# Kernel optimization log

Measured on AMD Instinct MI355X. Metric: run time of the kernel, lower is better.

Reference implementation:

```python
import jax, jax.numpy as jnp
import numpy as np

N, E, F_IN, H, C = 50000, 800000, 128, 4, 32
NEG_SLOPE = 0.2
BN_EPS = 1e-5


def setup_inputs() -> dict:
    key = jax.random.key(0)
    ks = jax.random.split(key, 6)
    x = jax.random.normal(ks[0], (N, F_IN), dtype=jnp.float32)
    edge_index = jax.random.randint(ks[1], (2, E), 0, N, dtype=jnp.int64)
    W = jax.random.normal(ks[2], (H * C, F_IN), dtype=jnp.float32) * (1.0 / np.sqrt(F_IN))
    att_src = jax.random.normal(ks[3], (H, C), dtype=jnp.float32) * 0.1
    att_dst = jax.random.normal(ks[4], (H, C), dtype=jnp.float32) * 0.1
    bias = jnp.zeros((H * C,), dtype=jnp.float32)
    gamma = jnp.ones((H * C,), dtype=jnp.float32)
    beta = jnp.zeros((H * C,), dtype=jnp.float32)
    return {"x": x, "edge_index": edge_index, "W": W, "att_src": att_src,
            "att_dst": att_dst, "bias": bias, "gamma": gamma, "beta": beta}


def reference(x, edge_index, W, att_src, att_dst, bias, gamma, beta):
    n = x.shape[0]
    loop = jnp.arange(n, dtype=edge_index.dtype)
    src = jnp.concatenate([edge_index[0], loop])  # add_self_loops=True (PyG default)
    dst = jnp.concatenate([edge_index[1], loop])
    # Linear projection (lin has no bias in GATConv)
    h = (x @ W.T).reshape(n, H, C)                      # [N,H,C]
    a_src = jnp.einsum('nhc,hc->nh', h, att_src)        # [N,H]
    a_dst = jnp.einsum('nhc,hc->nh', h, att_dst)
    e = jax.nn.leaky_relu(a_src[src] + a_dst[dst], NEG_SLOPE)  # [E+N,H]
    # segment softmax over incoming edges of each dst node
    emax = jax.ops.segment_max(e, dst, num_segments=n)
    emax = jnp.where(jnp.isfinite(emax), emax, 0.0)
    ex = jnp.exp(e - emax[dst])
    denom = jax.ops.segment_sum(ex, dst, num_segments=n)
    alpha = ex / (denom[dst] + 1e-16)                   # [E+N,H]
    msg = h[src] * alpha[:, :, None]                    # [E+N,H,C]
    out = jax.ops.segment_sum(msg, dst, num_segments=n).reshape(n, H * C) + bias
    out = jax.nn.relu(out)
    # BatchNorm1d over node dimension (training-mode batch stats)
    mean = out.mean(axis=0)
    var = out.var(axis=0)
    out = (out - mean) * jax.lax.rsqrt(var + BN_EPS) * gamma + beta
    return out
```

## Files before the change

kernel.cpp:

```cpp
#include <hip/hip_runtime.h>
#include <hip/hip_bf16.h>

#define HEADS 4
#define FDIM 128
#define NEG_SLOPE 0.2f
#define BN_EPS 1e-5f
#define CAP 3072
#define NB 512
#define NSLOT 32

typedef __attribute__((ext_vector_type(8))) short s8v;
typedef __attribute__((ext_vector_type(4))) float f4v;

__device__ __forceinline__ float lrelu(float x) { return x >= 0.f ? x : NEG_SLOPE * x; }

__device__ __forceinline__ unsigned short f2bf(float f) {
    unsigned int u = __float_as_uint(f);
    unsigned int r = (u + 0x7fffu + ((u >> 16) & 1u)) >> 16;
    return (unsigned short)r;
}
__device__ __forceinline__ float bflo(unsigned int u) { return __uint_as_float(u << 16); }
__device__ __forceinline__ float bfhi(unsigned int u) { return __uint_as_float(u & 0xffff0000u); }

__global__ __launch_bounds__(256) void k1_gemm_count(
    const float* __restrict__ x, const float* __restrict__ W,
    const float* __restrict__ att_src, const float* __restrict__ att_dst,
    const int* __restrict__ ei,
    unsigned short* __restrict__ hb, float* __restrict__ a_src,
    float* __restrict__ a_dst, int* __restrict__ cnts,
    int n, int E, int nbuk, int cpb, int gb)
{
    __shared__ uint4 bsh[2048];
    __shared__ int shi[512];
    int t = threadIdx.x;

    if ((int)blockIdx.x >= gb) {
        int cbid = blockIdx.x - gb;
        for (int i = t; i < nbuk; i += 256) shi[i] = 0;
        __syncthreads();
        int e0 = cbid * cpb, e1 = min(E, e0 + cpb);
        for (int e = e0 + t; e < e1; e += 256) atomicAdd(&shi[ei[E + e] >> 7], 1);
        __syncthreads();
        for (int i = t; i < nbuk; i += 256) cnts[cbid * nbuk + i] = shi[i];
        return;
    }

    for (int i = t; i < 2048; i += 256) {
        int l = i & 63, kt = (i >> 6) & 3, nt = i >> 8;
        int nrow = nt * 16 + (l & 15);
        int kb = kt * 32 + ((l >> 4) << 3);
        const float* src = W + nrow * FDIM + kb;
        float4 f0 = *(const float4*)src, f1 = *(const float4*)(src + 4);
        unsigned u0 = f2bf(f0.x) | ((unsigned)f2bf(f0.y) << 16);
        unsigned u1 = f2bf(f0.z) | ((unsigned)f2bf(f0.w) << 16);
        unsigned u2 = f2bf(f1.x) | ((unsigned)f2bf(f1.y) << 16);
        unsigned u3 = f2bf(f1.z) | ((unsigned)f2bf(f1.w) << 16);
        bsh[i] = make_uint4(u0, u1, u2, u3);
    }
    __syncthreads();

    int l = t & 63, wid = t >> 6;
    int r_base = blockIdx.x * 64 + wid * 16;
    int rg = l >> 4, l15 = l & 15;
    int row_in = r_base + l15;
    int rd = row_in < n ? row_in : 0;

    f4v acc[8];
#pragma unroll
    for (int i = 0; i < 8; ++i) acc[i] = (f4v){0.f, 0.f, 0.f, 0.f};
#pragma unroll
    for (int kt = 0; kt < 4; ++kt) {
        const float4* xp = (const float4*)(x + (size_t)rd * FDIM + kt * 32 + (rg << 3));
        float4 f0 = xp[0], f1 = xp[1];
        s8v a;
        a[0] = (short)f2bf(f0.x); a[1] = (short)f2bf(f0.y);
        a[2] = (short)f2bf(f0.z); a[3] = (short)f2bf(f0.w);
        a[4] = (short)f2bf(f1.x); a[5] = (short)f2bf(f1.y);
        a[6] = (short)f2bf(f1.z); a[7] = (short)f2bf(f1.w);
#pragma unroll
        for (int nt = 0; nt < 8; ++nt) {
            s8v b = *(const s8v*)&bsh[(nt * 4 + kt) * 64 + l];
            acc[nt] = __builtin_amdgcn_mfma_f32_16x16x32_bf16(a, b, acc[nt], 0, 0, 0);
        }
    }

    float asv[8], adv[8];
#pragma unroll
    for (int nt = 0; nt < 8; ++nt) {
        asv[nt] = att_src[nt * 16 + l15];
        adv[nt] = att_dst[nt * 16 + l15];
    }
#pragma unroll
    for (int r = 0; r < 4; ++r) {
        int row = r_base + rg * 4 + r;
        float ps[HEADS], pd[HEADS];
#pragma unroll
        for (int h = 0; h < HEADS; ++h) {
            ps[h] = acc[2 * h][r] * asv[2 * h] + acc[2 * h + 1][r] * asv[2 * h + 1];
            pd[h] = acc[2 * h][r] * adv[2 * h] + acc[2 * h + 1][r] * adv[2 * h + 1];
        }
#pragma unroll
        for (int d = 1; d < 16; d <<= 1) {
#pragma unroll
            for (int h = 0; h < HEADS; ++h) {
                ps[h] += __shfl_xor(ps[h], d);
                pd[h] += __shfl_xor(pd[h], d);
            }
        }
        if (l15 == 0 && row < n) {
            *(float4*)&a_src[row * HEADS] = make_float4(ps[0], ps[1], ps[2], ps[3]);
            *(float4*)&a_dst[row * HEADS] = make_float4(pd[0], pd[1], pd[2], pd[3]);
        }
    }
#pragma unroll
    for (int nt = 0; nt < 8; ++nt) {
#pragma unroll
        for (int r = 0; r < 4; ++r) {
            int row = r_base + rg * 4 + r;
            if (row < n) hb[(size_t)row * FDIM + nt * 16 + l15] = f2bf(acc[nt][r]);
        }
    }
}

__global__ __launch_bounds__(256) void k2_scanblk(const int* __restrict__ cnts,
                                                  int* __restrict__ bases,
                                                  int* __restrict__ sizes, int nbuk) {
    __shared__ int tmp[512];
    int b = blockIdx.x, t = threadIdx.x;
    int v0 = cnts[t * nbuk + b];
    int v1 = cnts[(t + 256) * nbuk + b];
    tmp[t] = v0; tmp[t + 256] = v1;
    __syncthreads();
    for (int s = 1; s < 512; s <<= 1) {
        int x0 = (t >= s) ? tmp[t - s] : 0;
        int x1 = (t + 256 >= s) ? tmp[t + 256 - s] : 0;
        __syncthreads();
        tmp[t] += x0; tmp[t + 256] += x1;
        __syncthreads();
    }
    bases[t * nbuk + b] = tmp[t] - v0;
    bases[(t + 256) * nbuk + b] = tmp[t + 256] - v1;
    if (t == 255) sizes[b] = tmp[511];
}

__global__ __launch_bounds__(1024) void k3_bucket_scan(
    const int* __restrict__ ei, const int* __restrict__ bases,
    const int* __restrict__ sizes, unsigned int* __restrict__ bucketed,
    int* __restrict__ goffs, int* __restrict__ offs,
    float* __restrict__ slotbuf,
    int N, int E, int nbuk, int cpb)
{
    __shared__ int lb[512];
    __shared__ int lr[512];
    int t = threadIdx.x;
    if ((int)blockIdx.x == NB) {
        int v = 0;
        if (t < 512) { v = (t < nbuk) ? sizes[t] : 0; lb[t] = v; }
        __syncthreads();
        for (int s = 1; s < 512; s <<= 1) {
            int x = (t < 512 && t >= s) ? lb[t - s] : 0;
            __syncthreads();
            if (t < 512) lb[t] += x;
            __syncthreads();
        }
        if (t < nbuk) goffs[t] = lb[t] - v;
        if (t == 0) { goffs[nbuk] = E; offs[N] = E; }
        for (int i = t; i < NSLOT * 256; i += 1024) slotbuf[i] = 0.f;
        return;
    }
    int bid = blockIdx.x;
    for (int i = t; i < nbuk; i += 1024) { lb[i] = bases[bid * nbuk + i]; lr[i] = 0; }
    __syncthreads();
    int e0 = bid * cpb, e1 = min(E, e0 + cpb);
    for (int e = e0 + t; e < e1; e += 1024) {
        int s = ei[e], d = ei[E + e];
        int b = d >> 7;
        int r = atomicAdd(&lr[b], 1);
        int p = lb[b] + r;
        if (p < CAP)
            bucketed[(size_t)b * CAP + p] = ((unsigned)(d & 127) << 16) | (unsigned)s;
    }
}

__global__ __launch_bounds__(256) void k4_csr(const unsigned int* __restrict__ bucketed,
                                              const int* __restrict__ sizes,
                                              const int* __restrict__ goffs,
                                              int* __restrict__ offs,
                                              unsigned short* __restrict__ csr, int N) {
    __shared__ int cnt[512], loff[512], tmp[512];
    int b = blockIdx.x, t = threadIdx.x;
    int sz = min(sizes[b], CAP), gbase = goffs[b];
    cnt[t] = 0; cnt[t + 256] = 0;
    __syncthreads();
    const unsigned int* seg = bucketed + (size_t)b * CAP;
    for (int j = t; j < sz; j += 256) {
        unsigned rec = seg[j];
        int key = (int)((rec >> 16) << 2) | (int)((rec & 0xffffu) >> 14);
        atomicAdd(&cnt[key], 1);
    }
    __syncthreads();
    tmp[t] = cnt[t]; tmp[t + 256] = cnt[t + 256];
    __syncthreads();
    for (int s = 1; s < 512; s <<= 1) {
        int x0 = (t >= s) ? tmp[t - s] : 0;
        int x1 = (t + 256 >= s) ? tmp[t + 256 - s] : 0;
        __syncthreads();
        tmp[t] += x0; tmp[t + 256] += x1;
        __syncthreads();
    }
    loff[t] = tmp[t] - cnt[t];
    loff[t + 256] = tmp[t + 256] - cnt[t + 256];
    if (t < 128) {
        int node = b * 128 + t;
        if (node < N) offs[node] = gbase + tmp[4 * t] - cnt[4 * t];
    }
    __syncthreads();
    for (int j = t; j < sz; j += 256) {
        unsigned rec = seg[j];
        int src = (int)(rec & 0xffffu);
        int key = (int)((rec >> 16) << 2) | (src >> 14);
        int pos = atomicAdd(&loff[key], 1);
        csr[gbase + pos] = (unsigned short)src;
    }
}

#define AGG_E(S, EW)                                                         \
    {                                                                        \
        uint4 u_ = *(const uint4*)&hb[(size_t)(S) * FDIM + c8];              \
        acc0.x += (EW) * bflo(u_.x); acc0.y += (EW) * bfhi(u_.x);            \
        acc0.z += (EW) * bflo(u_.y); acc0.w += (EW) * bfhi(u_.y);            \
        acc1.x += (EW) * bflo(u_.z); acc1.y += (EW) * bfhi(u_.z);            \
        acc1.z += (EW) * bflo(u_.w); acc1.w += (EW) * bfhi(u_.w);            \
        denom += (EW);                                                       \
    }

#define ACC2(E0, U0, E1, U1)                                                 \
    acc0.x += (E0) * bflo((U0).x) + (E1) * bflo((U1).x);                     \
    acc0.y += (E0) * bfhi((U0).x) + (E1) * bfhi((U1).x);                     \
    acc0.z += (E0) * bflo((U0).y) + (E1) * bflo((U1).y);                     \
    acc0.w += (E0) * bfhi((U0).y) + (E1) * bfhi((U1).y);                     \
    acc1.x += (E0) * bflo((U0).z) + (E1) * bflo((U1).z);                     \
    acc1.y += (E0) * bfhi((U0).z) + (E1) * bfhi((U1).z);                     \
    acc1.z += (E0) * bflo((U0).w) + (E1) * bflo((U1).w);                     \
    acc1.w += (E0) * bfhi((U0).w) + (E1) * bfhi((U1).w);

__global__ __launch_bounds__(256) void k5_agg(
    const unsigned short* __restrict__ hb, const float* __restrict__ a_src,
    const float* __restrict__ a_dst, const int* __restrict__ offs,
    const unsigned short* __restrict__ csr, const float* __restrict__ bias,
    unsigned short* __restrict__ outb, int n)
{
    int lane = threadIdx.x & 63;
    int node = blockIdx.x * 4 + (threadIdx.x >> 6);
    if (node >= n) return;
    int g = lane >> 4;
    int q = lane & 15;
    int c8 = q * 8;
    int head = q >> 2;

    float ad = a_dst[node * HEADS + head];
    int beg = offs[node], end = offs[node + 1];

    float4 acc0 = make_float4(0.f, 0.f, 0.f, 0.f);
    float4 acc1 = make_float4(0.f, 0.f, 0.f, 0.f);
    float denom = 0.f;

    if (g == 0) {
        float e_ = __expf(lrelu(a_src[node * HEADS + head] + ad));
        AGG_E(node, e_);
    }

    int j = beg + g;
    for (; j + 12 < end; j += 16) {
        int s0 = csr[j], s1 = csr[j + 4], s2 = csr[j + 8], s3 = csr[j + 12];
        float A0 = a_src[s0 * HEADS + head];
        float A1 = a_src[s1 * HEADS + head];
        float A2 = a_src[s2 * HEADS + head];
        float A3 = a_src[s3 * HEADS + head];
        uint4 u0 = *(const uint4*)&hb[(size_t)s0 * FDIM + c8];
        uint4 u1 = *(const uint4*)&hb[(size_t)s1 * FDIM + c8];
        uint4 u2 = *(const uint4*)&hb[(size_t)s2 * FDIM + c8];
        uint4 u3 = *(const uint4*)&hb[(size_t)s3 * FDIM + c8];
        float e0 = __expf(lrelu(A0 + ad));
        float e1 = __expf(lrelu(A1 + ad));
        float e2 = __expf(lrelu(A2 + ad));
        float e3 = __expf(lrelu(A3 + ad));
        ACC2(e0, u0, e1, u1);
        ACC2(e2, u2, e3, u3);
        denom += e0 + e1 + e2 + e3;
    }
    for (; j + 4 < end; j += 8) {
        int s0 = csr[j], s1 = csr[j + 4];
        float A0 = a_src[s0 * HEADS + head];
        float A1 = a_src[s1 * HEADS + head];
        uint4 u0 = *(const uint4*)&hb[(size_t)s0 * FDIM + c8];
        uint4 u1 = *(const uint4*)&hb[(size_t)s1 * FDIM + c8];
        float e0 = __expf(lrelu(A0 + ad));
        float e1 = __expf(lrelu(A1 + ad));
        ACC2(e0, u0, e1, u1);
        denom += e0 + e1;
    }
    for (; j < end; j += 4) {
        int s0 = csr[j];
        float e0 = __expf(lrelu(a_src[s0 * HEADS + head] + ad));
        AGG_E(s0, e0);
    }

#pragma unroll
    for (int d = 16; d < 64; d <<= 1) {
        acc0.x += __shfl_xor(acc0.x, d);
        acc0.y += __shfl_xor(acc0.y, d);
        acc0.z += __shfl_xor(acc0.z, d);
        acc0.w += __shfl_xor(acc0.w, d);
        acc1.x += __shfl_xor(acc1.x, d);
        acc1.y += __shfl_xor(acc1.y, d);
        acc1.z += __shfl_xor(acc1.z, d);
        acc1.w += __shfl_xor(acc1.w, d);
        denom += __shfl_xor(denom, d);
    }

    if (g == 0) {
        float inv = 1.f / (denom + 1e-16f);
        float4 b0 = *(const float4*)&bias[c8];
        float4 b1 = *(const float4*)&bias[c8 + 4];
        float o0 = fmaxf(acc0.x * inv + b0.x, 0.f);
        float o1 = fmaxf(acc0.y * inv + b0.y, 0.f);
        float o2 = fmaxf(acc0.z * inv + b0.z, 0.f);
        float o3 = fmaxf(acc0.w * inv + b0.w, 0.f);
        float o4 = fmaxf(acc1.x * inv + b1.x, 0.f);
        float o5 = fmaxf(acc1.y * inv + b1.y, 0.f);
        float o6 = fmaxf(acc1.z * inv + b1.z, 0.f);
        float o7 = fmaxf(acc1.w * inv + b1.w, 0.f);
        uint4 p;
        p.x = (unsigned)f2bf(o0) | ((unsigned)f2bf(o1) << 16);
        p.y = (unsigned)f2bf(o2) | ((unsigned)f2bf(o3) << 16);
        p.z = (unsigned)f2bf(o4) | ((unsigned)f2bf(o5) << 16);
        p.w = (unsigned)f2bf(o6) | ((unsigned)f2bf(o7) << 16);
        ((uint4*)outb)[(size_t)node * 16 + q] = p;
    }
}

__global__ __launch_bounds__(256) void bn_sums(const unsigned short* __restrict__ outb,
                                               float* __restrict__ slotbuf, int n) {
    int t = threadIdx.x;
    int q = t & 31, rh = t >> 5;
    float4 s = make_float4(0.f, 0.f, 0.f, 0.f);
    float4 s2 = make_float4(0.f, 0.f, 0.f, 0.f);
    const uint2* o2 = (const uint2*)outb;
    for (int r = blockIdx.x * 8 + rh; r < n; r += gridDim.x * 8) {
        uint2 u = o2[(size_t)r * 32 + q];
        float4 v = make_float4(bflo(u.x), bfhi(u.x), bflo(u.y), bfhi(u.y));
        s.x += v.x; s.y += v.y; s.z += v.z; s.w += v.w;
        s2.x += v.x * v.x; s2.y += v.y * v.y; s2.z += v.z * v.z; s2.w += v.w * v.w;
    }
    __shared__ float4 sh[2][8][32];
    sh[0][rh][q] = s;
    sh[1][rh][q] = s2;
    __syncthreads();
    if (rh == 0) {
#pragma unroll
        for (int i = 1; i < 8; ++i) {
            float4 a = sh[0][i][q], b = sh[1][i][q];
            s.x += a.x; s.y += a.y; s.z += a.z; s.w += a.w;
            s2.x += b.x; s2.y += b.y; s2.z += b.z; s2.w += b.w;
        }
        float* slot = slotbuf + (blockIdx.x & (NSLOT - 1)) * 256;
        atomicAdd(&slot[q * 4 + 0], s.x);
        atomicAdd(&slot[q * 4 + 1], s.y);
        atomicAdd(&slot[q * 4 + 2], s.z);
        atomicAdd(&slot[q * 4 + 3], s.w);
        atomicAdd(&slot[128 + q * 4 + 0], s2.x);
        atomicAdd(&slot[128 + q * 4 + 1], s2.y);
        atomicAdd(&slot[128 + q * 4 + 2], s2.z);
        atomicAdd(&slot[128 + q * 4 + 3], s2.w);
    }
}

__global__ __launch_bounds__(256) void k6_bn_apply(
    float* __restrict__ out, const unsigned short* __restrict__ outb,
    const float* __restrict__ slotbuf,
    const float* __restrict__ gamma, const float* __restrict__ beta, int N)
{
    __shared__ __align__(16) float sc[FDIM], sh[FDIM];
    int t = threadIdx.x;
    if (t < FDIM) {
        float s = 0.f, s2 = 0.f;
#pragma unroll
        for (int k = 0; k < NSLOT; ++k) {
            s  += slotbuf[k * 256 + t];
            s2 += slotbuf[k * 256 + 128 + t];
        }
        float mean = s / (float)N;
        float var = fmaxf(s2 / (float)N - mean * mean, 0.f);
        float g = gamma[t] * rsqrtf(var + BN_EPS);
        sc[t] = g;
        sh[t] = beta[t] - mean * g;
    }
    __syncthreads();
    int n4 = N * 32;
    const uint2* o2 = (const uint2*)outb;
    for (int i = blockIdx.x * 256 + t; i < n4; i += gridDim.x * 256) {
        uint2 u = o2[i];
        float4 v = make_float4(bflo(u.x), bfhi(u.x), bflo(u.y), bfhi(u.y));
        int f = (i & 31) * 4;
        float4 s4 = *(const float4*)&sc[f];
        float4 h4 = *(const float4*)&sh[f];
        v.x = v.x * s4.x + h4.x;
        v.y = v.y * s4.y + h4.y;
        v.z = v.z * s4.z + h4.z;
        v.w = v.w * s4.w + h4.w;
        ((float4*)out)[i] = v;
    }
}

static inline size_t align256(size_t x) { return (x + 255) & ~(size_t)255; }

extern "C" void kernel_launch(void* const* d_in, const int* in_sizes, int n_in,
                              void* d_out, int out_size, void* d_ws, size_t ws_size,
                              hipStream_t stream) {
    const float* x       = (const float*)d_in[0];
    const int*   ei      = (const int*)d_in[1];
    const float* W       = (const float*)d_in[2];
    const float* att_src = (const float*)d_in[3];
    const float* att_dst = (const float*)d_in[4];
    const float* bias    = (const float*)d_in[5];
    const float* gamma   = (const float*)d_in[6];
    const float* beta    = (const float*)d_in[7];
    float* out = (float*)d_out;

    int N = in_sizes[0] / FDIM;
    int E = in_sizes[1] / 2;
    int nbuk = (N + 127) >> 7;
    int cpb = (E + NB - 1) / NB;
    int gb = (N + 63) / 64;

    char* w = (char*)d_ws;
    unsigned short* hb = (unsigned short*)w;  w += align256((size_t)N * FDIM * 2);
    float* a_src  = (float*)w;  w += align256((size_t)N * HEADS * 4);
    float* a_dst  = (float*)w;  w += align256((size_t)N * HEADS * 4);
    int*   offs   = (int*)w;    w += align256((size_t)(N + 1) * 4);
    int*   cnts   = (int*)w;    w += align256((size_t)NB * nbuk * 4);
    int*   bases  = (int*)w;    w += align256((size_t)NB * nbuk * 4);
    int*   sizes  = (int*)w;    w += align256((size_t)nbuk * 4);
    int*   goffs  = (int*)w;    w += align256((size_t)(nbuk + 1) * 4);
    unsigned int* bucketed = (unsigned int*)w;  w += align256((size_t)nbuk * CAP * 4);
    unsigned short* csr = (unsigned short*)w;   w += align256((size_t)E * 2);
    unsigned short* outb = (unsigned short*)w;  w += align256((size_t)N * FDIM * 2);
    float* slotbuf = (float*)w; w += align256((size_t)NSLOT * 256 * 4);

    k1_gemm_count<<<gb + NB, 256, 0, stream>>>(x, W, att_src, att_dst, ei,
                                               hb, a_src, a_dst, cnts,
                                               N, E, nbuk, cpb, gb);
    k2_scanblk<<<nbuk, 256, 0, stream>>>(cnts, bases, sizes, nbuk);
    k3_bucket_scan<<<NB + 1, 1024, 0, stream>>>(ei, bases, sizes, bucketed,
                                                goffs, offs, slotbuf,
                                                N, E, nbuk, cpb);
    k4_csr<<<nbuk, 256, 0, stream>>>(bucketed, sizes, goffs, offs, csr, N);
    k5_agg<<<(N + 3) / 4, 256, 0, stream>>>(hb, a_src, a_dst, offs, csr, bias, outb, N);
    bn_sums<<<512, 256, 0, stream>>>(outb, slotbuf, N);
    k6_bn_apply<<<2048, 256, 0, stream>>>(out, outb, slotbuf, gamma, beta, N);
}
```

Measured before the change: 97.96 us.

## Fuse BN statistics into aggregation, locally sort bucket scatter, simplify CSR build

The BatchNorm sum and sum-of-squares accumulation moves into the aggregation kernel through a shared-memory reduction plus slot atomics. This removes the separate bn_sums pass that re-read the output, and a tiny finalize kernel now computes scale and shift. The bucket scatter first sorts each block's edges by bucket in shared memory so global writes land contiguously. The CSR kernel now keys on destination node only (128 bins) rather than node plus source high bits, which shrinks its scan but drops the within-node ordering by source. NSLOT doubles to cut atomic contention, at the cost of 12500 blocks hitting atomics and a CSR order that may lose locality.

After: 116.5 us. +19.0%, slower.

```diff
diff --git a/kernel.cpp b/kernel.cpp
--- a/kernel.cpp
+++ b/kernel.cpp
@@ -7,7 +7,7 @@
 #define BN_EPS 1e-5f
 #define CAP 3072
 #define NB 512
-#define NSLOT 32
+#define NSLOT 64
 
 typedef __attribute__((ext_vector_type(8))) short s8v;
 typedef __attribute__((ext_vector_type(4))) float f4v;
@@ -151,7 +151,10 @@
     int N, int E, int nbuk, int cpb)
 {
     __shared__ int lb[512];
-    __shared__ int lr[512];
+    __shared__ int cnt[512];
+    __shared__ int bscan[512];
+    __shared__ int loff[512];
+    __shared__ unsigned recs[2048];
     int t = threadIdx.x;
     if ((int)blockIdx.x == NB) {
         int v = 0;
@@ -169,16 +172,45 @@
         return;
     }
     int bid = blockIdx.x;
-    for (int i = t; i < nbuk; i += 1024) { lb[i] = bases[bid * nbuk + i]; lr[i] = 0; }
+    if (t < 512) {
+        lb[t] = (t < nbuk) ? bases[bid * nbuk + t] : 0;
+        cnt[t] = 0;
+    }
     __syncthreads();
     int e0 = bid * cpb, e1 = min(E, e0 + cpb);
+    int szblk = e1 - e0;
+    unsigned myrec[2]; int myb[2]; int nmine = 0;
     for (int e = e0 + t; e < e1; e += 1024) {
         int s = ei[e], d = ei[E + e];
         int b = d >> 7;
-        int r = atomicAdd(&lr[b], 1);
-        int p = lb[b] + r;
+        myrec[nmine] = ((unsigned)b << 23) | ((unsigned)(d & 127) << 16) | (unsigned)s;
+        myb[nmine] = b;
+        ++nmine;
+        atomicAdd(&cnt[b], 1);
+    }
+    __syncthreads();
+    if (t < 512) bscan[t] = cnt[t];
+    __syncthreads();
+    for (int s = 1; s < 512; s <<= 1) {
+        int x = (t < 512 && t >= s) ? bscan[t - s] : 0;
+        __syncthreads();
+        if (t < 512) bscan[t] += x;
+        __syncthreads();
+    }
+    if (t < 512) loff[t] = bscan[t] - cnt[t];
+    __syncthreads();
+    for (int k = 0; k < nmine; ++k) {
+        int pos = atomicAdd(&loff[myb[k]], 1);
+        recs[pos] = myrec[k];
+    }
+    __syncthreads();
+    for (int i = t; i < szblk; i += 1024) {
+        unsigned rec = recs[i];
+        int b = rec >> 23;
+        int local = i - (bscan[b] - cnt[b]);
+        int p = lb[b] + local;
         if (p < CAP)
-            bucketed[(size_t)b * CAP + p] = ((unsigned)(d & 127) << 16) | (unsigned)s;
+            bucketed[(size_t)b * CAP + p] = rec & 0x7fffffu;
     }
 }
 
@@ -187,40 +219,33 @@
                                               const int* __restrict__ goffs,
                                               int* __restrict__ offs,
                                               unsigned short* __restrict__ csr, int N) {
-    __shared__ int cnt[512], loff[512], tmp[512];
+    __shared__ int cnt[128], loff[128], tmp[128];
     int b = blockIdx.x, t = threadIdx.x;
     int sz = min(sizes[b], CAP), gbase = goffs[b];
-    cnt[t] = 0; cnt[t + 256] = 0;
+    if (t < 128) cnt[t] = 0;
     __syncthreads();
     const unsigned int* seg = bucketed + (size_t)b * CAP;
+    for (int j = t; j < sz; j += 256) atomicAdd(&cnt[(seg[j] >> 16) & 127], 1);
+    __syncthreads();
+    if (t < 128) tmp[t] = cnt[t];
+    __syncthreads();
+    for (int s = 1; s < 128; s <<= 1) {
+        int x = (t < 128 && t >= s) ? tmp[t - s] : 0;
+        __syncthreads();
+        if (t < 128) tmp[t] += x;
+        __syncthreads();
+    }
+    if (t < 128) {
+        loff[t] = tmp[t] - cnt[t];
+        int node = b * 128 + t;
+        if (node < N) offs[node] = gbase + loff[t];
+    }
+    __syncthreads();
     for (int j = t; j < sz; j += 256) {
         unsigned rec = seg[j];
-        int key = (int)((rec >> 16) << 2) | (int)((rec & 0xffffu) >> 14);
-        atomicAdd(&cnt[key], 1);
-    }
-    __syncthreads();
-    tmp[t] = cnt[t]; tmp[t + 256] = cnt[t + 256];
-    __syncthreads();
-    for (int s = 1; s < 512; s <<= 1) {
-        int x0 = (t >= s) ? tmp[t - s] : 0;
-        int x1 = (t + 256 >= s) ? tmp[t + 256 - s] : 0;
-        __syncthreads();
-        tmp[t] += x0; tmp[t + 256] += x1;
-        __syncthreads();
-    }
-    loff[t] = tmp[t] - cnt[t];
-    loff[t + 256] = tmp[t + 256] - cnt[t + 256];
-    if (t < 128) {
-        int node = b * 128 + t;
-        if (node < N) offs[node] = gbase + tmp[4 * t] - cnt[4 * t];
-    }
-    __syncthreads();
-    for (int j = t; j < sz; j += 256) {
-        unsigned rec = seg[j];
-        int src = (int)(rec & 0xffffu);
-        int key = (int)((rec >> 16) << 2) | (src >> 14);
-        int pos = atomicAdd(&loff[key], 1);
-        csr[gbase + pos] = (unsigned short)src;
+        int nd = (rec >> 16) & 127;
+        int pos = atomicAdd(&loff[nd], 1);
+        csr[gbase + pos] = (unsigned short)(rec & 0xffffu);
     }
 }
 
@@ -248,153 +273,159 @@
     const unsigned short* __restrict__ hb, const float* __restrict__ a_src,
     const float* __restrict__ a_dst, const int* __restrict__ offs,
     const unsigned short* __restrict__ csr, const float* __restrict__ bias,
-    unsigned short* __restrict__ outb, int n)
+    unsigned short* __restrict__ outb, float* __restrict__ slotbuf, int n)
 {
-    int lane = threadIdx.x & 63;
-    int node = blockIdx.x * 4 + (threadIdx.x >> 6);
-    if (node >= n) return;
+    int t = threadIdx.x;
+    int lane = t & 63, wid = t >> 6;
+    int node = blockIdx.x * 4 + wid;
+    bool valid = node < n;
     int g = lane >> 4;
     int q = lane & 15;
     int c8 = q * 8;
     int head = q >> 2;
 
-    float ad = a_dst[node * HEADS + head];
-    int beg = offs[node], end = offs[node + 1];
-
-    float4 acc0 = make_float4(0.f, 0.f, 0.f, 0.f);
-    float4 acc1 = make_float4(0.f, 0.f, 0.f, 0.f);
-    float denom = 0.f;
-
+    float o0 = 0.f, o1 = 0.f, o2 = 0.f, o3 = 0.f;
+    float o4 = 0.f, o5 = 0.f, o6 = 0.f, o7 = 0.f;
+
+    if (valid) {
+        float ad = a_dst[node * HEADS + head];
+        int beg = offs[node], end = offs[node + 1];
+
+        float4 acc0 = make_float4(0.f, 0.f, 0.f, 0.f);
+        float4 acc1 = make_float4(0.f, 0.f, 0.f, 0.f);
+        float denom = 0.f;
+
+        if (g == 0) {
+            float e_ = __expf(lrelu(a_src[node * HEADS + head] + ad));
+            AGG_E(node, e_);
+        }
+
+        int j = beg + g;
+        for (; j + 12 < end; j += 16) {
+            int s0 = csr[j], s1 = csr[j + 4], s2 = csr[j + 8], s3 = csr[j + 12];
+            float A0 = a_src[s0 * HEADS + head];
+            float A1 = a_src[s1 * HEADS + head];
+            float A2 = a_src[s2 * HEADS + head];
+            float A3 = a_src[s3 * HEADS + head];
+            uint4 u0 = *(const uint4*)&hb[(size_t)s0 * FDIM + c8];
+            uint4 u1 = *(const uint4*)&hb[(size_t)s1 * FDIM + c8];
+            uint4 u2 = *(const uint4*)&hb[(size_t)s2 * FDIM + c8];
+            uint4 u3 = *(const uint4*)&hb[(size_t)s3 * FDIM + c8];
+            float e0 = __expf(lrelu(A0 + ad));
+            float e1 = __expf(lrelu(A1 + ad));
+            float e2 = __expf(lrelu(A2 + ad));
+            float e3 = __expf(lrelu(A3 + ad));
+            ACC2(e0, u0, e1, u1);
+            ACC2(e2, u2, e3, u3);
+            denom += e0 + e1 + e2 + e3;
+        }
+        for (; j + 4 < end; j += 8) {
+            int s0 = csr[j], s1 = csr[j + 4];
+            float A0 = a_src[s0 * HEADS + head];
+            float A1 = a_src[s1 * HEADS + head];
+            uint4 u0 = *(const uint4*)&hb[(size_t)s0 * FDIM + c8];
+            uint4 u1 = *(const uint4*)&hb[(size_t)s1 * FDIM + c8];
+            float e0 = __expf(lrelu(A0 + ad));
+            float e1 = __expf(lrelu(A1 + ad));
+            ACC2(e0, u0, e1, u1);
+            denom += e0 + e1;
+        }
+        for (; j < end; j += 4) {
+            int s0 = csr[j];
+            float e0 = __expf(lrelu(a_src[s0 * HEADS + head] + ad));
+            AGG_E(s0, e0);
+        }
+
+#pragma unroll
+        for (int d = 16; d < 64; d <<= 1) {
+            acc0.x += __shfl_xor(acc0.x, d);
+            acc0.y += __shfl_xor(acc0.y, d);
+            acc0.z += __shfl_xor(acc0.z, d);
+            acc0.w += __shfl_xor(acc0.w, d);
+            acc1.x += __shfl_xor(acc1.x, d);
+            acc1.y += __shfl_xor(acc1.y, d);
+            acc1.z += __shfl_xor(acc1.z, d);
+            acc1.w += __shfl_xor(acc1.w, d);
+            denom += __shfl_xor(denom, d);
+        }
+
+        if (g == 0) {
+            float inv = 1.f / (denom + 1e-16f);
+            float4 b0 = *(const float4*)&bias[c8];
+            float4 b1 = *(const float4*)&bias[c8 + 4];
+            o0 = fmaxf(acc0.x * inv + b0.x, 0.f);
+            o1 = fmaxf(acc0.y * inv + b0.y, 0.f);
+            o2 = fmaxf(acc0.z * inv + b0.z, 0.f);
+            o3 = fmaxf(acc0.w * inv + b0.w, 0.f);
+            o4 = fmaxf(acc1.x * inv + b1.x, 0.f);
+            o5 = fmaxf(acc1.y * inv + b1.y, 0.f);
+            o6 = fmaxf(acc1.z * inv + b1.z, 0.f);
+            o7 = fmaxf(acc1.w * inv + b1.w, 0.f);
+            uint4 p;
+            p.x = (unsigned)f2bf(o0) | ((unsigned)f2bf(o1) << 16);
+            p.y = (unsigned)f2bf(o2) | ((unsigned)f2bf(o3) << 16);
+            p.z = (unsigned)f2bf(o4) | ((unsigned)f2bf(o5) << 16);
+            p.w = (unsigned)f2bf(o6) | ((unsigned)f2bf(o7) << 16);
+            ((uint4*)outb)[(size_t)node * 16 + q] = p;
+        }
+    }
+
+    __shared__ float4 redS[4][16][2];
+    __shared__ float4 redQ[4][16][2];
     if (g == 0) {
-        float e_ = __expf(lrelu(a_src[node * HEADS + head] + ad));
-        AGG_E(node, e_);
-    }
-
-    int j = beg + g;
-    for (; j + 12 < end; j += 16) {
-        int s0 = csr[j], s1 = csr[j + 4], s2 = csr[j + 8], s3 = csr[j + 12];
-        float A0 = a_src[s0 * HEADS + head];
-        float A1 = a_src[s1 * HEADS + head];
-        float A2 = a_src[s2 * HEADS + head];
-        float A3 = a_src[s3 * HEADS + head];
-        uint4 u0 = *(const uint4*)&hb[(size_t)s0 * FDIM + c8];
-        uint4 u1 = *(const uint4*)&hb[(size_t)s1 * FDIM + c8];
-        uint4 u2 = *(const uint4*)&hb[(size_t)s2 * FDIM + c8];
-        uint4 u3 = *(const uint4*)&hb[(size_t)s3 * FDIM + c8];
-        float e0 = __expf(lrelu(A0 + ad));
-        float e1 = __expf(lrelu(A1 + ad));
-        float e2 = __expf(lrelu(A2 + ad));
-        float e3 = __expf(lrelu(A3 + ad));
-        ACC2(e0, u0, e1, u1);
-        ACC2(e2, u2, e3, u3);
-        denom += e0 + e1 + e2 + e3;
-    }
-    for (; j + 4 < end; j += 8) {
-        int s0 = csr[j], s1 = csr[j + 4];
-        float A0 = a_src[s0 * HEADS + head];
-        float A1 = a_src[s1 * HEADS + head];
-        uint4 u0 = *(const uint4*)&hb[(size_t)s0 * FDIM + c8];
-        uint4 u1 = *(const uint4*)&hb[(size_t)s1 * FDIM + c8];
-        float e0 = __expf(lrelu(A0 + ad));
-        float e1 = __expf(lrelu(A1 + ad));
-        ACC2(e0, u0, e1, u1);
-        denom += e0 + e1;
-    }
-    for (; j < end; j += 4) {
-        int s0 = csr[j];
-        float e0 = __expf(lrelu(a_src[s0 * HEADS + head] + ad));
-        AGG_E(s0, e0);
-    }
-
-#pragma unroll
-    for (int d = 16; d < 64; d <<= 1) {
-        acc0.x += __shfl_xor(acc0.x, d);
-        acc0.y += __shfl_xor(acc0.y, d);
-        acc0.z += __shfl_xor(acc0.z, d);
-        acc0.w += __shfl_xor(acc0.w, d);
-        acc1.x += __shfl_xor(acc1.x, d);
-        acc1.y += __shfl_xor(acc1.y, d);
-        acc1.z += __shfl_xor(acc1.z, d);
-        acc1.w += __shfl_xor(acc1.w, d);
-        denom += __shfl_xor(denom, d);
-    }
-
-    if (g == 0) {
-        float inv = 1.f / (denom + 1e-16f);
-        float4 b0 = *(const float4*)&bias[c8];
-        float4 b1 = *(const float4*)&bias[c8 + 4];
-        float o0 = fmaxf(acc0.x * inv + b0.x, 0.f);
-        float o1 = fmaxf(acc0.y * inv + b0.y, 0.f);
-        float o2 = fmaxf(acc0.z * inv + b0.z, 0.f);
-        float o3 = fmaxf(acc0.w * inv + b0.w, 0.f);
-        float o4 = fmaxf(acc1.x * inv + b1.x, 0.f);
-        float o5 = fmaxf(acc1.y * inv + b1.y, 0.f);
-        float o6 = fmaxf(acc1.z * inv + b1.z, 0.f);
-        float o7 = fmaxf(acc1.w * inv + b1.w, 0.f);
-        uint4 p;
-        p.x = (unsigned)f2bf(o0) | ((unsigned)f2bf(o1) << 16);
-        p.y = (unsigned)f2bf(o2) | ((unsigned)f2bf(o3) << 16);
-        p.z = (unsigned)f2bf(o4) | ((unsigned)f2bf(o5) << 16);
-        p.w = (unsigned)f2bf(o6) | ((unsigned)f2bf(o7) << 16);
-        ((uint4*)outb)[(size_t)node * 16 + q] = p;
-    }
-}
-
-__global__ __launch_bounds__(256) void bn_sums(const unsigned short* __restrict__ outb,
-                                               float* __restrict__ slotbuf, int n) {
+        redS[wid][q][0] = make_float4(o0, o1, o2, o3);
+        redS[wid][q][1] = make_float4(o4, o5, o6, o7);
+        redQ[wid][q][0] = make_float4(o0 * o0, o1 * o1, o2 * o2, o3 * o3);
+        redQ[wid][q][1] = make_float4(o4 * o4, o5 * o5, o6 * o6, o7 * o7);
+    }
+    __syncthreads();
+    if (t < 64) {
+        int qq = t >> 2, part = (t >> 1) & 1, which = t & 1;
+        float4 a = which ? redQ[0][qq][part] : redS[0][qq][part];
+        float4 b = which ? redQ[1][qq][part] : redS[1][qq][part];
+        float4 c = which ? redQ[2][qq][part] : redS[2][qq][part];
+        float4 d = which ? redQ[3][qq][part] : redS[3][qq][part];
+        float4 s;
+        s.x = a.x + b.x + c.x + d.x;
+        s.y = a.y + b.y + c.y + d.y;
+        s.z = a.z + b.z + c.z + d.z;
+        s.w = a.w + b.w + c.w + d.w;
+        int ch = qq * 8 + part * 4;
+        float* slot = slotbuf + (blockIdx.x & (NSLOT - 1)) * 256 + which * 128;
+        atomicAdd(&slot[ch + 0], s.x);
+        atomicAdd(&slot[ch + 1], s.y);
+        atomicAdd(&slot[ch + 2], s.z);
+        atomicAdd(&slot[ch + 3], s.w);
+    }
+}
+
+__global__ void bn_finalize(const float* __restrict__ slotbuf,
+                            const float* __restrict__ gamma,
+                            const float* __restrict__ beta,
+                            float* __restrict__ scsh, int N) {
     int t = threadIdx.x;
-    int q = t & 31, rh = t >> 5;
-    float4 s = make_float4(0.f, 0.f, 0.f, 0.f);
-    float4 s2 = make_float4(0.f, 0.f, 0.f, 0.f);
-    const uint2* o2 = (const uint2*)outb;
-    for (int r = blockIdx.x * 8 + rh; r < n; r += gridDim.x * 8) {
-        uint2 u = o2[(size_t)r * 32 + q];
-        float4 v = make_float4(bflo(u.x), bfhi(u.x), bflo(u.y), bfhi(u.y));
-        s.x += v.x; s.y += v.y; s.z += v.z; s.w += v.w;
-        s2.x += v.x * v.x; s2.y += v.y * v.y; s2.z += v.z * v.z; s2.w += v.w * v.w;
-    }
-    __shared__ float4 sh[2][8][32];
-    sh[0][rh][q] = s;
-    sh[1][rh][q] = s2;
-    __syncthreads();
-    if (rh == 0) {
-#pragma unroll
-        for (int i = 1; i < 8; ++i) {
-            float4 a = sh[0][i][q], b = sh[1][i][q];
-            s.x += a.x; s.y += a.y; s.z += a.z; s.w += a.w;
-            s2.x += b.x; s2.y += b.y; s2.z += b.z; s2.w += b.w;
-        }
-        float* slot = slotbuf + (blockIdx.x & (NSLOT - 1)) * 256;
-        atomicAdd(&slot[q * 4 + 0], s.x);
-        atomicAdd(&slot[q * 4 + 1], s.y);
-        atomicAdd(&slot[q * 4 + 2], s.z);
-        atomicAdd(&slot[q * 4 + 3], s.w);
-        atomicAdd(&slot[128 + q * 4 + 0], s2.x);
-        atomicAdd(&slot[128 + q * 4 + 1], s2.y);
-        atomicAdd(&slot[128 + q * 4 + 2], s2.z);
-        atomicAdd(&slot[128 + q * 4 + 3], s2.w);
-    }
+    float s = 0.f, s2 = 0.f;
+#pragma unroll
+    for (int k = 0; k < NSLOT; ++k) {
+        s  += slotbuf[k * 256 + t];
+        s2 += slotbuf[k * 256 + 128 + t];
+    }
+    float mean = s / (float)N;
+    float var = fmaxf(s2 / (float)N - mean * mean, 0.f);
+    float g = gamma[t] * rsqrtf(var + BN_EPS);
+    scsh[t] = g;
+    scsh[128 + t] = beta[t] - mean * g;
 }
 
 __global__ __launch_bounds__(256) void k6_bn_apply(
     float* __restrict__ out, const unsigned short* __restrict__ outb,
-    const float* __restrict__ slotbuf,
-    const float* __restrict__ gamma, const float* __restrict__ beta, int N)
+    const float* __restrict__ scsh, int N)
 {
     __shared__ __align__(16) float sc[FDIM], sh[FDIM];
     int t = threadIdx.x;
     if (t < FDIM) {
-        float s = 0.f, s2 = 0.f;
-#pragma unroll
-        for (int k = 0; k < NSLOT; ++k) {
-            s  += slotbuf[k * 256 + t];
-            s2 += slotbuf[k * 256 + 128 + t];
-        }
-        float mean = s / (float)N;
-        float var = fmaxf(s2 / (float)N - mean * mean, 0.f);
-        float g = gamma[t] * rsqrtf(var + BN_EPS);
-        sc[t] = g;
-        sh[t] = beta[t] - mean * g;
+        sc[t] = scsh[t];
+        sh[t] = scsh[128 + t];
     }
     __syncthreads();
     int n4 = N * 32;
@@ -447,6 +478,7 @@
     unsigned short* csr = (unsigned short*)w;   w += align256((size_t)E * 2);
     unsigned short* outb = (unsigned short*)w;  w += align256((size_t)N * FDIM * 2);
     float* slotbuf = (float*)w; w += align256((size_t)NSLOT * 256 * 4);
+    float* scsh    = (float*)w; w += align256((size_t)256 * 4);
 
     k1_gemm_count<<<gb + NB, 256, 0, stream>>>(x, W, att_src, att_dst, ei,
                                                hb, a_src, a_dst, cnts,
@@ -456,7 +488,8 @@
                                                 goffs, offs, slotbuf,
                                                 N, E, nbuk, cpb);
     k4_csr<<<nbuk, 256, 0, stream>>>(bucketed, sizes, goffs, offs, csr, N);
-    k5_agg<<<(N + 3) / 4, 256, 0, stream>>>(hb, a_src, a_dst, offs, csr, bias, outb, N);
-    bn_sums<<<512, 256, 0, stream>>>(outb, slotbuf, N);
-    k6_bn_apply<<<2048, 256, 0, stream>>>(out, outb, slotbuf, gamma, beta, N);
-}
+    k5_agg<<<(N + 3) / 4, 256, 0, stream>>>(hb, a_src, a_dst, offs, csr, bias,
+                                            outb, slotbuf, N);
+    bn_finalize<<<1, 128, 0, stream>>>(slotbuf, gamma, beta, scsh, N);
+    k6_bn_apply<<<2048, 256, 0, stream>>>(out, outb, scsh, N);
+}
```
